# Kernel optimization log

Measured on AMD Instinct MI355X. Metric: run time of the kernel, lower is better.

Reference implementation:

```python
import jax, jax.numpy as jnp
import numpy as np

N = 100000   # nodes
E = 1600000  # edges (before self-loops)
D = 128      # in_feats
H = 128      # n_hidden


def setup_inputs() -> dict:
    key = jax.random.key(0)
    k = jax.random.split(key, 6)
    x = jax.random.normal(k[0], (N, D), dtype=jnp.float32)
    src = jax.random.randint(k[1], (E,), 0, N, dtype=jnp.int32)
    dst = jax.random.randint(k[2], (E,), 0, N, dtype=jnp.int32)
    W1 = jax.random.normal(k[3], (D, H), dtype=jnp.float32) / np.float32(np.sqrt(D))
    b1 = jnp.zeros((H,), jnp.float32)
    W2 = jax.random.normal(k[4], (H, H), dtype=jnp.float32) / np.float32(np.sqrt(H))
    b2 = jnp.zeros((H,), jnp.float32)
    return {"x": x, "src": src, "dst": dst, "W1": W1, "b1": b1, "W2": W2, "b2": b2}


def _gcn(x, src, dst, W1, b1, W2, b2):
    n = x.shape[0]
    # add_self_loop(g)
    loops = jnp.arange(n, dtype=src.dtype)
    s = jnp.concatenate([src, loops])
    d = jnp.concatenate([dst, loops])
    ones = jnp.ones((s.shape[0],), dtype=x.dtype)
    deg_out = jax.ops.segment_sum(ones, s, num_segments=n)  # src out-degree
    deg_in = jax.ops.segment_sum(ones, d, num_segments=n)   # dst in-degree
    # DGL GraphConv norm='both': D_out^{-1/2} on source side, D_in^{-1/2} on dest side
    norm_out = jax.lax.rsqrt(jnp.maximum(deg_out, 1.0))[:, None]
    norm_in = jax.lax.rsqrt(jnp.maximum(deg_in, 1.0))[:, None]

    def layer(h, W, b):
        h = h * norm_out                                   # [n, f]
        agg = jax.ops.segment_sum(h[s], d, num_segments=n)  # gather + scatter-add over edges
        return (agg * norm_in) @ W + b

    h = layer(x, W1, b1)
    # dropout p=0 -> identity
    h = layer(h, W2, b2)
    return h


def reference(x, src, dst, W1, b1, W2, b2):
    return _gcn(x, src, dst, W1, b1, W2, b2)
```

## Files before the change

### kernel.cpp

```cpp
#include <hip/hip_runtime.h>

#define FD 128
#define SHIFT 10
#define BNODES 1024
#define NBK 128
#define CHUNK 4096
#define ST 512

typedef unsigned int u32;
typedef unsigned short u16;
typedef unsigned char u8;
typedef __attribute__((ext_vector_type(8))) short short8;
typedef __attribute__((ext_vector_type(4))) float f32x4;
typedef __attribute__((ext_vector_type(4))) u32 u32x4;

__device__ inline u16 f2bf(float f) {
  u32 u = __float_as_uint(f);
  u += 0x7fffu + ((u >> 16) & 1u);
  return (u16)(u >> 16);
}
__device__ inline float bf2f(u16 h) { return __uint_as_float((u32)h << 16); }

__global__ __launch_bounds__(512) void k_histpw(
    const int* __restrict__ src, const int* __restrict__ dst,
    int* __restrict__ bcntD, int* __restrict__ bcntS, int e, int n, int nbuck,
    const float* __restrict__ W1, u32* __restrict__ wf1hi, u32* __restrict__ wf1lo,
    const float* __restrict__ W2, u32* __restrict__ wf2hi, u32* __restrict__ wf2lo) {
  int tid = threadIdx.x;
  if (blockIdx.x >= 256) {
    int gi = (blockIdx.x - 256) * 512 + tid;
    int i = gi & 8191;
    const float* W = (gi < 8192) ? W1 : W2;
    u32* wfhi = (gi < 8192) ? wf1hi : wf2hi;
    u32* wflo = (gi < 8192) ? wf1lo : wf2lo;
    int m = i & 3, l = (i >> 2) & 63, f = i >> 8;
    int kt = f & 3, nt = f >> 2;
    int k0 = kt * 32 + ((l >> 4) << 3) + 2 * m;
    int c = nt * 16 + (l & 15);
    float w0 = W[k0 * FD + c], w1 = W[(k0 + 1) * FD + c];
    u16 h0 = f2bf(w0), h1 = f2bf(w1);
    u16 l0 = f2bf(w0 - bf2f(h0)), l1 = f2bf(w1 - bf2f(h1));
    wfhi[i] = (u32)h0 | ((u32)h1 << 16);
    wflo[i] = (u32)l0 | ((u32)l1 << 16);
    return;
  }
  __shared__ int shD[NBK];
  __shared__ int shS[NBK];
  if (tid < NBK) { shD[tid] = 0; shS[tid] = 0; }
  __syncthreads();
  int total = e + n;
  for (int t = blockIdx.x * 512 + tid; t < total; t += 256 * 512) {
    if (t < e) {
      atomicAdd(&shD[dst[t] >> SHIFT], 1);
      atomicAdd(&shS[src[t] >> SHIFT], 1);
    } else {
      atomicAdd(&shD[(t - e) >> SHIFT], 1);
    }
  }
  __syncthreads();
  if (tid < nbuck) {
    if (shD[tid]) atomicAdd(&bcntD[tid], shD[tid]);
    if (shS[tid]) atomicAdd(&bcntS[tid], shS[tid]);
  }
}

__global__ __launch_bounds__(NBK) void k_bscan(
    const int* __restrict__ bcntD, const int* __restrict__ bcntS,
    int* __restrict__ bbaseD, int* __restrict__ bcurD,
    int* __restrict__ bbaseS, int* __restrict__ bcurS,
    int nbuck, int totalD, int totalS) {
  __shared__ int shD[NBK];
  __shared__ int shS[NBK];
  int tid = threadIdx.x;
  int vD = (tid < nbuck) ? bcntD[tid] : 0;
  int vS = (tid < nbuck) ? bcntS[tid] : 0;
  shD[tid] = vD; shS[tid] = vS;
  __syncthreads();
  for (int off = 1; off < NBK; off <<= 1) {
    int aD = (tid >= off) ? shD[tid - off] : 0;
    int aS = (tid >= off) ? shS[tid - off] : 0;
    __syncthreads();
    shD[tid] += aD; shS[tid] += aS;
    __syncthreads();
  }
  if (tid < nbuck) {
    int exD = shD[tid] - vD; bbaseD[tid] = exD; bcurD[tid] = exD;
    int exS = shS[tid] - vS; bbaseS[tid] = exS; bcurS[tid] = exS;
  }
  if (tid == 0) { bbaseD[nbuck] = totalD; bbaseS[nbuck] = totalS; }
}

__global__ __launch_bounds__(ST) void k_scatgx(
    const int* __restrict__ src, const int* __restrict__ dst,
    int* __restrict__ bcurD, int* __restrict__ bcurS,
    u32* __restrict__ pairs, u16* __restrict__ pairs2,
    int e, int n, int nbuck, int nsc,
    const float* __restrict__ x,
    const u32* __restrict__ wfhi, const u32* __restrict__ wflo,
    u32* __restrict__ tout) {
  __shared__ __align__(16) u8 smem[36864];
  int tid512 = threadIdx.x;

  if (blockIdx.x >= (unsigned)nsc) {
    int u = tid512 >> 8, tid = tid512 & 255;
    u32* Au = (u32*)smem + u * 4096;
    int lane = tid & 63;
    int mt = tid >> 6;
    int r0 = ((blockIdx.x - nsc) * 2 + u) * 64;

    #pragma unroll
    for (int it = 0; it < 16; ++it) {
      int w = it * 256 + tid;
      int row = w >> 6, uu = w & 63;
      int grow = r0 + row;
      float2 v = make_float2(0.f, 0.f);
      if (grow < n) v = *(const float2*)(x + (size_t)grow * FD + uu * 2);
      Au[row * 64 + (uu ^ ((row & 7) << 2))] = (u32)f2bf(v.x) | ((u32)f2bf(v.y) << 16);
    }
    __syncthreads();

    short8 afh[4];
    int arow = mt * 16 + (lane & 15);
    #pragma unroll
    for (int kt = 0; kt < 4; ++kt) {
      int boff = arow * 256 + ((kt * 64 + (lane >> 4) * 16) ^ ((arow & 7) << 4));
      afh[kt] = *(const short8*)((const char*)Au + boff);
    }
    __syncthreads();

    for (int nt = 0; nt < 8; ++nt) {
      f32x4 oacc = {0.f, 0.f, 0.f, 0.f};
      #pragma unroll
      for (int kt = 0; kt < 4; ++kt) {
        int f = nt * 4 + kt;
        short8 wh = *(const short8*)(wfhi + (size_t)(f * 64 + lane) * 4);
        short8 wl = *(const short8*)(wflo + (size_t)(f * 64 + lane) * 4);
        oacc = __builtin_amdgcn_mfma_f32_16x16x32_bf16(afh[kt], wh, oacc, 0, 0, 0);
        oacc = __builtin_amdgcn_mfma_f32_16x16x32_bf16(afh[kt], wl, oacc, 0, 0, 0);
      }
      int c = nt * 16 + (lane & 15);
      #pragma unroll
      for (int j = 0; j < 4; ++j) {
        int lrow = mt * 16 + (lane >> 4) * 4 + j;
        ((u16*)Au)[lrow * 128 + c] = f2bf(oacc[j]);
      }
    }
    __syncthreads();
    #pragma unroll
    for (int it = 0; it < 4; ++it) {
      int ci = it * 256 + tid;
      int lrow = ci >> 4, chk = ci & 15;
      int row = r0 + lrow;
      if (row < n)
        *(u32x4*)(tout + (size_t)row * 64 + chk * 4) =
            *(const u32x4*)(Au + lrow * 64 + chk * 4);
    }
    return;
  }

  int* histD = (int*)smem;
  int* exclD = histD + NBK;
  int* gbaseD = exclD + NBK;
  int* rankD = gbaseD + NBK;
  int* histS = rankD + NBK;
  int* exclS = histS + NBK;
  int* gbaseS = exclS + NBK;
  int* rankS = gbaseS + NBK;
  u32* stgv = (u32*)(smem + 4096);
  u16* stg2 = (u16*)(smem + 20480);
  u8*  stgb = smem + 28672;
  u8*  stg2b = smem + 32768;
  int tid = tid512;
  int c0 = blockIdx.x * CHUNK;
  int total = e + n;
  if (tid < NBK) { histD[tid] = 0; histS[tid] = 0; }
  __syncthreads();
  u32 pv_[8]; int bD_[8], bS_[8]; bool v_[8], vs_[8];
  #pragma unroll
  for (int i = 0; i < 8; ++i) {
    int t = c0 + i * ST + tid;
    v_[i] = (t < total);
    vs_[i] = (t < e);
    pv_[i] = 0; bD_[i] = 0; bS_[i] = 0;
    if (v_[i]) {
      int s, d;
      if (vs_[i]) { s = src[t]; d = dst[t]; }
      else        { s = t - e;  d = s; }
      pv_[i] = ((u32)(d & (BNODES - 1)) << 22) | (u32)s;
      bD_[i] = d >> SHIFT;
      atomicAdd(&histD[bD_[i]], 1);
      if (vs_[i]) { bS_[i] = s >> SHIFT; atomicAdd(&histS[bS_[i]], 1); }
    }
  }
  __syncthreads();
  int hD = 0, hS = 0;
  if (tid < NBK) { hD = histD[tid]; hS = histS[tid]; }
  __syncthreads();
  for (int off = 1; off < NBK; off <<= 1) {
    int aD = 0, aS = 0;
    if (tid < NBK && tid >= off) { aD = histD[tid - off]; aS = histS[tid - off]; }
    __syncthreads();
    if (tid < NBK) { histD[tid] += aD; histS[tid] += aS; }
    __syncthreads();
  }
  if (tid < NBK) {
    int exD = histD[tid] - hD; exclD[tid] = exD; rankD[tid] = exD;
    int exS = histS[tid] - hS; exclS[tid] = exS; rankS[tid] = exS;
    gbaseD[tid] = (tid < nbuck && hD > 0) ? atomicAdd(&bcurD[tid], hD) : 0;
    gbaseS[tid] = (tid < nbuck && hS > 0) ? atomicAdd(&bcurS[tid], hS) : 0;
  }
  __syncthreads();
  #pragma unroll
  for (int i = 0; i < 8; ++i) {
    if (v_[i]) {
      int p = atomicAdd(&rankD[bD_[i]], 1);
      stgv[p] = pv_[i];
      stgb[p] = (u8)bD_[i];
    }
    if (vs_[i]) {
      int p = atomicAdd(&rankS[bS_[i]], 1);
      stg2[p] = (u16)(pv_[i] & (BNODES - 1));
      stg2b[p] = (u8)bS_[i];
    }
  }
  __syncthreads();
  int V = min(CHUNK, total - c0);
  for (int j = tid; j < V; j += ST) {
    int b = stgb[j];
    pairs[gbaseD[b] + (j - exclD[b])] = stgv[j];
  }
  int V2 = min(CHUNK, e - c0);
  for (int j = tid; j < V2; j += ST) {
    int b = stg2b[j];
    pairs2[gbaseS[b] + (j - exclS[b])] = stg2[j];
  }
}

__global__ __launch_bounds__(1024) void k_build(
    const u32* __restrict__ pairs, const int* __restrict__ bbase,
    const u16* __restrict__ pairs2, const int* __restrict__ bbaseS,
    int* __restrict__ rp, int* __restrict__ col,
    float* __restrict__ nin, float* __restrict__ nout,
    int n, int nbuck, int total) {
  __shared__ int cnt[BNODES];
  __shared__ int cur[BNODES];
  __shared__ int wsum[16];
  int tid = threadIdx.x;
  if (blockIdx.x >= (unsigned)nbuck) {
    int b = blockIdx.x - nbuck;
    int base = bbaseS[b], end = bbaseS[b + 1];
    cnt[tid] = 0;
    __syncthreads();
    for (int t = base + tid; t < end; t += 1024)
      atomicAdd(&cnt[(int)pairs2[t]], 1);
    __syncthreads();
    int node = (b << SHIFT) + tid;
    if (node < n) nout[node] = rsqrtf((float)(cnt[tid] + 1));
    return;
  }
  int b = blockIdx.x;
  int base = bbase[b], end = bbase[b + 1];
  int node0 = b << SHIFT;
  cnt[tid] = 0;
  __syncthreads();
  for (int t = base + tid; t < end; t += 1024)
    atomicAdd(&cnt[(int)(pairs[t] >> 22)], 1);
  __syncthreads();
  int c = cnt[tid];
  int lane = tid & 63, wv = tid >> 6;
  int v = c;
  #pragma unroll
  for (int o = 1; o < 64; o <<= 1) {
    int t = __shfl_up(v, o, 64);
    if (lane >= o) v += t;
  }
  if (lane == 63) wsum[wv] = v;
  __syncthreads();
  if (tid < 16) {
    int w = wsum[tid];
    #pragma unroll
    for (int o = 1; o < 16; o <<= 1) {
      int t = __shfl_up(w, o, 64);
      if (lane >= o) w += t;
    }
    wsum[tid] = w;
  }
  __syncthreads();
  int incl = v + (wv ? wsum[wv - 1] : 0);
  int ex = incl - c;
  int node = node0 + tid;
  if (node < n) {
    rp[node] = base + ex;
    nin[node] = rsqrtf((float)c);
  }
  if (b == nbuck - 1 && tid == 0) rp[n] = total;
  cur[tid] = ex;
  __syncthreads();
  for (int t = base + tid; t < end; t += 1024) {
    u32 pr = pairs[t];
    int p = atomicAdd(&cur[(int)(pr >> 22)], 1);
    col[base + p] = (int)(pr & 0x3FFFFFu);
  }
}

__global__ __launch_bounds__(256) void k_scale(
    const u32* __restrict__ t1, const float* __restrict__ nout,
    u32* __restrict__ y1, int n) {
  int tot = (n + 1) * 64;
  for (int idx = blockIdx.x * blockDim.x + threadIdx.x; idx < tot;
       idx += gridDim.x * blockDim.x) {
    int row = idx >> 6;
    if (row >= n) { y1[idx] = 0; continue; }
    float w = nout[row];
    u32 v = t1[idx];
    float lo = __uint_as_float(v << 16) * w;
    float hi = __uint_as_float(v & 0xFFFF0000u) * w;
    y1[idx] = (u32)f2bf(lo) | ((u32)f2bf(hi) << 16);
  }
}

__global__ __launch_bounds__(256) void k_agg(
    const u32* __restrict__ hs, const int* __restrict__ rp,
    const int* __restrict__ col, const float* __restrict__ nin,
    const float* __restrict__ bias,
    float* __restrict__ fout, u32* __restrict__ hsout, int n, int mode) {
  int wid = (blockIdx.x * 256 + threadIdx.x) >> 6;
  int lane = threadIdx.x & 63;
  int g = lane >> 4, ch = lane & 15;
  int r = wid * 4 + g;
  bool valid = (r < n);
  int e0 = 0, e1 = 0;
  if (valid) { e0 = rp[r]; e1 = rp[r + 1]; }
  int m = e1 - e0;
  m = max(m, __shfl_xor(m, 16, 64));
  m = max(m, __shfl_xor(m, 32, 64));
  int trips = (m + 7) >> 3;
  float acc[8] = {0.f, 0.f, 0.f, 0.f, 0.f, 0.f, 0.f, 0.f};
  const u32x4* hv = (const u32x4*)hs;
  int em1 = (e1 > 0) ? (e1 - 1) : 0;
  for (int it = 0; it < trips; ++it) {
    int tb = e0 + it * 8;
    u32x4 buf[8];
    #pragma unroll
    for (int u = 0; u < 8; ++u) {
      int idx = tb + u;
      int s = col[min(idx, em1)];
      s = (idx < e1) ? s : n;
      buf[u] = hv[(size_t)s * 16 + ch];
    }
    #pragma unroll
    for (int u = 0; u < 8; ++u)
      #pragma unroll
      for (int j = 0; j < 4; ++j) {
        u32 x = buf[u][j];
        acc[2 * j]     += __uint_as_float(x << 16);
        acc[2 * j + 1] += __uint_as_float(x & 0xFFFF0000u);
      }
  }
  if (!valid) return;
  float wi = nin[r];
  float4 b0 = *(const float4*)(bias + ch * 8);
  float4 b1v = *(const float4*)(bias + ch * 8 + 4);
  float v[8];
  v[0] = acc[0] * wi + b0.x;  v[1] = acc[1] * wi + b0.y;
  v[2] = acc[2] * wi + b0.z;  v[3] = acc[3] * wi + b0.w;
  v[4] = acc[4] * wi + b1v.x; v[5] = acc[5] * wi + b1v.y;
  v[6] = acc[6] * wi + b1v.z; v[7] = acc[7] * wi + b1v.w;
  if (mode == 0) {
    *(float4*)(fout + (size_t)r * FD + ch * 8)     = make_float4(v[0], v[1], v[2], v[3]);
    *(float4*)(fout + (size_t)r * FD + ch * 8 + 4) = make_float4(v[4], v[5], v[6], v[7]);
  } else {
    u32 hi[4];
    #pragma unroll
    for (int j = 0; j < 4; ++j)
      hi[j] = (u32)f2bf(v[2 * j]) | ((u32)f2bf(v[2 * j + 1]) << 16);
    int sch = ch ^ (r & 7);
    u32x4 hq = {hi[0], hi[1], hi[2], hi[3]};
    *(u32x4*)(hsout + (size_t)r * 64 + sch * 4) = hq;
  }
}

__global__ __launch_bounds__(256) void k_gemm2(
    const u32* __restrict__ ahi,
    const u32* __restrict__ wfhi, const u32* __restrict__ wflo,
    const float* __restrict__ nout, u32* __restrict__ yout, int n) {
  __shared__ u32 As[4096];
  int tid = threadIdx.x;
  int lane = tid & 63;
  int mt = tid >> 6;
  int r0 = blockIdx.x * 64;

  const u32x4* gh = (const u32x4*)(ahi + (size_t)r0 * 64);
  u32x4* sh_ = (u32x4*)As;
  #pragma unroll
  for (int t = 0; t < 4; ++t) sh_[t * 256 + tid] = gh[t * 256 + tid];
  __syncthreads();

  short8 afh[4];
  int arow = mt * 16 + (lane & 15);
  #pragma unroll
  for (int kt = 0; kt < 4; ++kt) {
    int boff = arow * 256 + ((kt * 64 + (lane >> 4) * 16) ^ ((arow & 7) << 4));
    afh[kt] = *(const short8*)((const char*)As + boff);
  }
  __syncthreads();

  float wout[4];
  #pragma unroll
  for (int j = 0; j < 4; ++j) {
    int row = r0 + mt * 16 + (lane >> 4) * 4 + j;
    wout[j] = (row < n) ? nout[row] : 0.f;
  }

  for (int nt = 0; nt < 8; ++nt) {
    f32x4 oacc = {0.f, 0.f, 0.f, 0.f};
    #pragma unroll
    for (int kt = 0; kt < 4; ++kt) {
      int f = nt * 4 + kt;
      short8 wh = *(const short8*)(wfhi + (size_t)(f * 64 + lane) * 4);
      short8 wl = *(const short8*)(wflo + (size_t)(f * 64 + lane) * 4);
      oacc = __builtin_amdgcn_mfma_f32_16x16x32_bf16(afh[kt], wh, oacc, 0, 0, 0);
      oacc = __builtin_amdgcn_mfma_f32_16x16x32_bf16(afh[kt], wl, oacc, 0, 0, 0);
    }
    int c = nt * 16 + (lane & 15);
    #pragma unroll
    for (int j = 0; j < 4; ++j) {
      int lrow = mt * 16 + (lane >> 4) * 4 + j;
      ((u16*)As)[lrow * 128 + c] = f2bf(oacc[j] * wout[j]);
    }
  }
  __syncthreads();
  #pragma unroll
  for (int it = 0; it < 4; ++it) {
    int ci = it * 256 + tid;
    int lrow = ci >> 4, chk = ci & 15;
    int row = r0 + lrow;
    if (row < n)
      *(u32x4*)(yout + (size_t)row * 64 + chk * 4) =
          *(const u32x4*)(As + lrow * 64 + chk * 4);
  }
}

extern "C" void kernel_launch(void* const* d_in, const int* in_sizes, int n_in,
                              void* d_out, int out_size, void* d_ws, size_t ws_size,
                              hipStream_t stream) {
  const float* x  = (const float*)d_in[0];
  const int* src  = (const int*)d_in[1];
  const int* dst  = (const int*)d_in[2];
  const float* W1 = (const float*)d_in[3];
  const float* b1 = (const float*)d_in[4];
  const float* W2 = (const float*)d_in[5];
  const float* b2 = (const float*)d_in[6];
  float* out = (float*)d_out;

  int n = in_sizes[0] / FD;
  int e = in_sizes[1];
  int total = e + n;
  int nbuck = (n + BNODES - 1) >> SHIFT;

  char* ws = (char*)d_ws;
  size_t off = 0;
  auto alloc = [&](size_t bytes) -> void* {
    void* p = ws + off;
    off += (bytes + 255) / 256 * 256;
    return p;
  };
  u32* bufA  = (u32*)alloc((size_t)(n + 16) * 64 * 4);
  u32* t1bf  = bufA;
  u32* y2    = bufA;
  u32* bufB  = (u32*)alloc((size_t)(n + 16) * 64 * 4);
  u32* pairs = bufB;
  u32* y1    = bufB;
  u32* bufC  = (u32*)alloc((size_t)(n + 64) * 64 * 4);
  u16* pairs2 = (u16*)bufC;
  u32* h1bf  = bufC;
  int* col   = (int*)alloc((size_t)total * 4 + 256);
  int* rp    = (int*)alloc((size_t)(n + 1) * 4);
  float* nin  = (float*)alloc((size_t)n * 4);
  float* nout = (float*)alloc((size_t)n * 4);
  int* bcntD  = (int*)alloc(NBK * 4);
  int* bcntS  = (int*)alloc(NBK * 4);
  int* bbaseD = (int*)alloc((NBK + 1) * 4);
  int* bbaseS = (int*)alloc((NBK + 1) * 4);
  int* bcurD  = (int*)alloc(NBK * 4);
  int* bcurS  = (int*)alloc(NBK * 4);
  u32* wf1hi  = (u32*)alloc(8192 * 4);
  u32* wf1lo  = (u32*)alloc(8192 * 4);
  u32* wf2hi  = (u32*)alloc(8192 * 4);
  u32* wf2lo  = (u32*)alloc(8192 * 4);

  hipMemsetAsync(bcntD, 0, (size_t)NBK * 4 * 2, stream);
  hipMemsetAsync(bufA + (size_t)n * 64, 0, 64 * 4, stream);

  k_histpw<<<288, 512, 0, stream>>>(src, dst, bcntD, bcntS, e, n, nbuck,
                                    W1, wf1hi, wf1lo, W2, wf2hi, wf2lo);
  k_bscan<<<1, NBK, 0, stream>>>(bcntD, bcntS, bbaseD, bcurD, bbaseS, bcurS,
                                 nbuck, total, e);
  int nsc = (total + CHUNK - 1) / CHUNK;
  int ngx = (n + 127) / 128;
  k_scatgx<<<nsc + ngx, ST, 0, stream>>>(src, dst, bcurD, bcurS, pairs, pairs2,
                                         e, n, nbuck, nsc, x, wf1hi, wf1lo, t1bf);
  k_build<<<2 * nbuck, 1024, 0, stream>>>(pairs, bbaseD, pairs2, bbaseS,
                                          rp, col, nin, nout, n, nbuck, total);
  k_scale<<<2048, 256, 0, stream>>>(t1bf, nout, y1, n);

  int agrid = (n + 15) / 16;
  int ggrid = (n + 63) / 64;
  k_agg<<<agrid, 256, 0, stream>>>(y1, rp, col, nin, b1, nullptr, h1bf, n, 1);
  k_gemm2<<<ggrid, 256, 0, stream>>>(h1bf, wf2hi, wf2lo, nout, y2, n);
  k_agg<<<agrid, 256, 0, stream>>>(y2, rp, col, nin, b2, out, nullptr, n, 0);
}
```

Before: 232.7 us.

## Fold source-norm scaling into layer-1 aggregation and enlarge edge scatter chunks

Removes the separate k_scale pass, which read the bf16 X·W1 rows, multiplied by the per-source out-degree norm and wrote them back. Instead the first aggregation loads nout[s] for each gathered edge and applies it with an FMA. A zeroed nout[n] sentinel covers padding edges. The edge bucketing kernel now processes 8192 edges per block with 16 items per thread. Its shared staging buffers are reused sequentially for the dst and src scatters, and pairs gets its own buffer. This trades a full-matrix read/write pass for one extra scalar gather per edge in layer 1, plus higher register and LDS use in the scatter kernel.

```diff
diff --git a/kernel.cpp b/kernel.cpp
--- a/kernel.cpp
+++ b/kernel.cpp
@@ -4,8 +4,9 @@
 #define SHIFT 10
 #define BNODES 1024
 #define NBK 128
-#define CHUNK 4096
+#define CHUNK 8192
 #define ST 512
+#define NIT 16
 
 typedef unsigned int u32;
 typedef unsigned short u16;
@@ -98,7 +99,7 @@
     const float* __restrict__ x,
     const u32* __restrict__ wfhi, const u32* __restrict__ wflo,
     u32* __restrict__ tout) {
-  __shared__ __align__(16) u8 smem[36864];
+  __shared__ __align__(16) u8 smem[45056];
   int tid512 = threadIdx.x;
 
   if (blockIdx.x >= (unsigned)nsc) {
@@ -167,17 +168,17 @@
   int* gbaseS = exclS + NBK;
   int* rankS = gbaseS + NBK;
   u32* stgv = (u32*)(smem + 4096);
-  u16* stg2 = (u16*)(smem + 20480);
-  u8*  stgb = smem + 28672;
-  u8*  stg2b = smem + 32768;
+  u8*  stgb = smem + 36864;
+  u16* stg2 = (u16*)(smem + 4096);
+  u8*  stg2b = smem + 20480;
   int tid = tid512;
   int c0 = blockIdx.x * CHUNK;
   int total = e + n;
   if (tid < NBK) { histD[tid] = 0; histS[tid] = 0; }
   __syncthreads();
-  u32 pv_[8]; int bD_[8], bS_[8]; bool v_[8], vs_[8];
-  #pragma unroll
-  for (int i = 0; i < 8; ++i) {
+  u32 pv_[NIT]; int bD_[NIT], bS_[NIT]; bool v_[NIT], vs_[NIT];
+  #pragma unroll
+  for (int i = 0; i < NIT; ++i) {
     int t = c0 + i * ST + tid;
     v_[i] = (t < total);
     vs_[i] = (t < e);
@@ -211,12 +212,22 @@
   }
   __syncthreads();
   #pragma unroll
-  for (int i = 0; i < 8; ++i) {
+  for (int i = 0; i < NIT; ++i) {
     if (v_[i]) {
       int p = atomicAdd(&rankD[bD_[i]], 1);
       stgv[p] = pv_[i];
       stgb[p] = (u8)bD_[i];
     }
+  }
+  __syncthreads();
+  int V = min(CHUNK, total - c0);
+  for (int j = tid; j < V; j += ST) {
+    int b = stgb[j];
+    pairs[gbaseD[b] + (j - exclD[b])] = stgv[j];
+  }
+  __syncthreads();
+  #pragma unroll
+  for (int i = 0; i < NIT; ++i) {
     if (vs_[i]) {
       int p = atomicAdd(&rankS[bS_[i]], 1);
       stg2[p] = (u16)(pv_[i] & (BNODES - 1));
@@ -224,11 +235,6 @@
     }
   }
   __syncthreads();
-  int V = min(CHUNK, total - c0);
-  for (int j = tid; j < V; j += ST) {
-    int b = stgb[j];
-    pairs[gbaseD[b] + (j - exclD[b])] = stgv[j];
-  }
   int V2 = min(CHUNK, e - c0);
   for (int j = tid; j < V2; j += ST) {
     int b = stg2b[j];
@@ -250,6 +256,7 @@
     int b = blockIdx.x - nbuck;
     int base = bbaseS[b], end = bbaseS[b + 1];
     cnt[tid] = 0;
+    if (b == 0 && tid == 0) nout[n] = 0.f;
     __syncthreads();
     for (int t = base + tid; t < end; t += 1024)
       atomicAdd(&cnt[(int)pairs2[t]], 1);
@@ -303,26 +310,10 @@
   }
 }
 
-__global__ __launch_bounds__(256) void k_scale(
-    const u32* __restrict__ t1, const float* __restrict__ nout,
-    u32* __restrict__ y1, int n) {
-  int tot = (n + 1) * 64;
-  for (int idx = blockIdx.x * blockDim.x + threadIdx.x; idx < tot;
-       idx += gridDim.x * blockDim.x) {
-    int row = idx >> 6;
-    if (row >= n) { y1[idx] = 0; continue; }
-    float w = nout[row];
-    u32 v = t1[idx];
-    float lo = __uint_as_float(v << 16) * w;
-    float hi = __uint_as_float(v & 0xFFFF0000u) * w;
-    y1[idx] = (u32)f2bf(lo) | ((u32)f2bf(hi) << 16);
-  }
-}
-
 __global__ __launch_bounds__(256) void k_agg(
     const u32* __restrict__ hs, const int* __restrict__ rp,
     const int* __restrict__ col, const float* __restrict__ nin,
-    const float* __restrict__ bias,
+    const float* __restrict__ snorm, const float* __restrict__ bias,
     float* __restrict__ fout, u32* __restrict__ hsout, int n, int mode) {
   int wid = (blockIdx.x * 256 + threadIdx.x) >> 6;
   int lane = threadIdx.x & 63;
@@ -341,21 +332,25 @@
   for (int it = 0; it < trips; ++it) {
     int tb = e0 + it * 8;
     u32x4 buf[8];
+    float wb[8];
     #pragma unroll
     for (int u = 0; u < 8; ++u) {
       int idx = tb + u;
       int s = col[min(idx, em1)];
       s = (idx < e1) ? s : n;
       buf[u] = hv[(size_t)s * 16 + ch];
-    }
-    #pragma unroll
-    for (int u = 0; u < 8; ++u)
+      if (mode) wb[u] = snorm[s];
+    }
+    #pragma unroll
+    for (int u = 0; u < 8; ++u) {
+      float w = mode ? wb[u] : 1.0f;
       #pragma unroll
       for (int j = 0; j < 4; ++j) {
         u32 x = buf[u][j];
-        acc[2 * j]     += __uint_as_float(x << 16);
-        acc[2 * j + 1] += __uint_as_float(x & 0xFFFF0000u);
+        acc[2 * j]     = fmaf(__uint_as_float(x << 16), w, acc[2 * j]);
+        acc[2 * j + 1] = fmaf(__uint_as_float(x & 0xFFFF0000u), w, acc[2 * j + 1]);
       }
+    }
   }
   if (!valid) return;
   float wi = nin[r];
@@ -468,16 +463,14 @@
   u32* bufA  = (u32*)alloc((size_t)(n + 16) * 64 * 4);
   u32* t1bf  = bufA;
   u32* y2    = bufA;
-  u32* bufB  = (u32*)alloc((size_t)(n + 16) * 64 * 4);
-  u32* pairs = bufB;
-  u32* y1    = bufB;
+  u32* pairs = (u32*)alloc((size_t)total * 4 + 256);
   u32* bufC  = (u32*)alloc((size_t)(n + 64) * 64 * 4);
   u16* pairs2 = (u16*)bufC;
   u32* h1bf  = bufC;
   int* col   = (int*)alloc((size_t)total * 4 + 256);
   int* rp    = (int*)alloc((size_t)(n + 1) * 4);
   float* nin  = (float*)alloc((size_t)n * 4);
-  float* nout = (float*)alloc((size_t)n * 4);
+  float* nout = (float*)alloc((size_t)(n + 16) * 4);
   int* bcntD  = (int*)alloc(NBK * 4);
   int* bcntS  = (int*)alloc(NBK * 4);
   int* bbaseD = (int*)alloc((NBK + 1) * 4);
@@ -502,11 +495,12 @@
                                          e, n, nbuck, nsc, x, wf1hi, wf1lo, t1bf);
   k_build<<<2 * nbuck, 1024, 0, stream>>>(pairs, bbaseD, pairs2, bbaseS,
                                           rp, col, nin, nout, n, nbuck, total);
-  k_scale<<<2048, 256, 0, stream>>>(t1bf, nout, y1, n);
 
   int agrid = (n + 15) / 16;
   int ggrid = (n + 63) / 64;
-  k_agg<<<agrid, 256, 0, stream>>>(y1, rp, col, nin, b1, nullptr, h1bf, n, 1);
+  k_agg<<<agrid, 256, 0, stream>>>(t1bf, rp, col, nin, nout, b1,
+                                   nullptr, h1bf, n, 1);
   k_gemm2<<<ggrid, 256, 0, stream>>>(h1bf, wf2hi, wf2lo, nout, y2, n);
-  k_agg<<<agrid, 256, 0, stream>>>(y2, rp, col, nin, b2, out, nullptr, n, 0);
-}
+  k_agg<<<agrid, 256, 0, stream>>>(y2, rp, col, nin, nullptr, b2,
+                                   out, nullptr, n, 0);
+}
```

New measurement: 258.9 us. 11.3% more time.
